# Kernel tuning notes

Measured on AMD Instinct MI355X. Metric: run time of the kernel, lower is better.

## Reference

```python
import jax, jax.numpy as jnp
import numpy as np

X, Y, Z, E, K, ITERS = 128, 128, 8, 64, 3, 3
XYZ = X * Y * Z
IMG_H, IMG_W = 384, 1280
FH, FW = 96, 320  # img_feat spatial size
LN_EPS = 1e-5
GRAD_SCALE = 0.1


def _homo_grid():
    # get_coordinates: meshgrid(arange(x), -arange(y), arange(z)), then append ones
    xs = (np.arange(X) * 0.8 + 0.0).astype(np.float32)
    ys = (-(np.arange(Y) * 0.8 - 51.2)).astype(np.float32)
    zs = (np.arange(Z) * 0.5 - 2.5).astype(np.float32)
    gx, gy, gz = np.meshgrid(xs, ys, zs, indexing='ij')
    g = np.stack([gx, gy, gz, np.ones_like(gx)], axis=-1)  # (X,Y,Z,4)
    return jnp.asarray(g)


def _grid_sample(img, grid):
    # F.grid_sample: bilinear, padding_mode='zeros', align_corners=False
    # img: (B,C,H,W), grid: (B,N,K,2) xy in [-1,1] -> out (B,C,N,K)
    B, C, H, W = img.shape
    x = ((grid[..., 0] + 1.0) * W - 1.0) * 0.5
    y = ((grid[..., 1] + 1.0) * H - 1.0) * 0.5
    x0 = jnp.floor(x); y0 = jnp.floor(y)
    x1 = x0 + 1.0; y1 = y0 + 1.0
    wx1 = x - x0; wx0 = 1.0 - wx1
    wy1 = y - y0; wy0 = 1.0 - wy1
    flat = img.reshape(B, C, H * W)

    def gather(xi, yi):
        valid = (xi >= 0) & (xi < W) & (yi >= 0) & (yi < H)  # (B,N,K)
        xi_c = jnp.clip(xi, 0, W - 1).astype(jnp.int32)
        yi_c = jnp.clip(yi, 0, H - 1).astype(jnp.int32)
        idx = yi_c * W + xi_c  # (B,N,K)
        g = jnp.take_along_axis(flat, idx.reshape(B, 1, -1), axis=2)
        g = g.reshape(B, C, idx.shape[1], idx.shape[2])
        return g * valid[:, None].astype(img.dtype)

    out = (gather(x0, y0) * (wx0 * wy0)[:, None]
           + gather(x1, y0) * (wx1 * wy0)[:, None]
           + gather(x0, y1) * (wx0 * wy1)[:, None]
           + gather(x1, y1) * (wx1 * wy1)[:, None])
    return out


def setup_inputs() -> dict:
    key = jax.random.key(0)
    ks = jax.random.split(key, 8)
    # realistic extrinsic (velo->cam) and intrinsic so projections land in-image
    T_velo2cam = jnp.array([[[0., -1., 0., 0.],
                             [0., 0., -1., -0.3],
                             [1., 0., 0., 0.5]]], dtype=jnp.float32)
    intrinsic = jnp.array([[[700., 0., 640.],
                            [0., 700., 192.],
                            [0., 0., 1.]]], dtype=jnp.float32)
    img_feat = jax.random.normal(ks[0], (1, E, FH, FW), jnp.float32)
    bev_embedding = 0.1 * jax.random.normal(ks[1], (X, Y, Z, E), jnp.float32)
    W_off = 0.02 * jax.random.normal(ks[2], (ITERS, E, 2 * K), jnp.float32)
    b_off = 0.02 * jax.random.normal(ks[3], (ITERS, 2 * K), jnp.float32)
    s_off = jnp.full((ITERS,), 0.1, jnp.float32)  # Scale(0.1)
    W_w = 0.02 * jax.random.normal(ks[4], (ITERS, E, K), jnp.float32)
    b_w = jnp.zeros((ITERS, K), jnp.float32)
    W_l = (E ** -0.5) * jax.random.normal(ks[5], (ITERS, E, E), jnp.float32)
    b_l = jnp.zeros((ITERS, E), jnp.float32)
    ln_g = jnp.ones((ITERS, E), jnp.float32)
    ln_b = jnp.zeros((ITERS, E), jnp.float32)
    return dict(T_velo2cam=T_velo2cam, intrinsic=intrinsic, img_feat=img_feat,
                bev_embedding=bev_embedding, W_off=W_off, b_off=b_off, s_off=s_off,
                W_w=W_w, b_w=b_w, W_l=W_l, b_l=b_l, ln_g=ln_g, ln_b=ln_b)


def reference(T_velo2cam, intrinsic, img_feat, bev_embedding,
              W_off, b_off, s_off, W_w, b_w, W_l, b_l, ln_g, ln_b):
    homo = _homo_grid()  # (X,Y,Z,4)
    T = jnp.einsum('bij,bjk->bik', intrinsic, T_velo2cam)  # (B,3,4)
    pts = jnp.einsum('bij,xyzj->bxyzi', T, homo)  # (B,X,Y,Z,3)
    uv = pts[..., 0:2] / pts[..., 2:3]
    half = jnp.array([IMG_W / 2.0, IMG_H / 2.0], pts.dtype)
    coord = (uv / half - 1.0).reshape(1, XYZ, 1, 2)  # (B,XYZ,1,2)
    bev = bev_embedding.reshape(1, XYZ, 1, E)
    for i in range(ITERS):
        off = (bev @ W_off[i] + b_off[i]) * s_off[i]  # Linear -> Scale
        # GradientScale(0.1): identity fwd, grad*0.1 bwd
        off = GRAD_SCALE * off + jax.lax.stop_gradient((1.0 - GRAD_SCALE) * off)
        off = off.reshape(1, XYZ, K, 2)
        w = jax.nn.softmax(bev @ W_w[i] + b_w[i], axis=-1)[:, :, 0, :]  # (1,XYZ,K)
        feat = _grid_sample(img_feat, coord + off)  # (1,E,XYZ,K)
        feat = jnp.sum(feat * w[:, None], axis=-1)  # (1,E,XYZ)
        bev = bev + jnp.transpose(feat, (0, 2, 1))[:, :, None, :]  # (1,XYZ,1,E)
        # LinearLNDropout (dropout inactive in eval)
        h = bev @ W_l[i] + b_l[i]
        mu = jnp.mean(h, axis=-1, keepdims=True)
        var = jnp.mean((h - mu) ** 2, axis=-1, keepdims=True)
        h = (h - mu) * jax.lax.rsqrt(var + LN_EPS) * ln_g[i] + ln_b[i]
        bev = bev + h
    bev = bev.reshape(1, X, Y, Z, E)
    return jnp.transpose(bev, (0, 4, 2, 1, 3)).mean(-1)  # (B,E,Y,X)
```

## Files before the change

### kernel.cpp

```cpp
#include <hip/hip_runtime.h>
#include <math.h>

#define XD 128
#define YD 128
#define ZD 8
#define ED 64
#define KD 3
#define NITER 3
#define FHD 96
#define FWD 320
#define HALF_W 640.0f
#define HALF_H 192.0f

#define ASTRIDE 80
#define DSTR 28
#define HSTRIDE 68

#define OFF_AB   0
#define OFF_SD   2560
#define OFF_SW   3328
#define OFF_DH   4096
#define OFF_CXY  8448
#define WAVE_LDS 8576

typedef __attribute__((ext_vector_type(8))) short short8;
typedef __attribute__((ext_vector_type(4))) float f32x4;

__device__ __forceinline__ unsigned short f2bf(float f) {
    unsigned u = __float_as_uint(f);
    u += 0x7fff + ((u >> 16) & 1);
    return (unsigned short)(u >> 16);
}

__global__ __launch_bounds__(256) void k_prep(const float* __restrict__ img,
                                              float* __restrict__ outHWC,
                                              const float* __restrict__ W_off,
                                              const float* __restrict__ W_w,
                                              const float* __restrict__ W_l,
                                              unsigned short* __restrict__ W9f,
                                              unsigned short* __restrict__ Wlf) {
    if (blockIdx.x < (FHD * FWD) / 64) {
        __shared__ float tile[64][65];
        const int hw0 = blockIdx.x * 64;
        const int lane = threadIdx.x & 63;
        const int r = threadIdx.x >> 6;
#pragma unroll
        for (int i = 0; i < 16; ++i) {
            int e = r + 4 * i;
            tile[e][lane] = img[e * (FHD * FWD) + hw0 + lane];
        }
        __syncthreads();
#pragma unroll
        for (int i = 0; i < 16; ++i) {
            int row = r + 4 * i;
            outHWC[(hw0 + row) * 64 + lane] = tile[lane][row];
        }
    } else {
        int idx = (blockIdx.x - (FHD * FWD) / 64) * 256 + threadIdx.x;
        if (idx < 3 * 4 * 2 * 64) {
            int lane = idx & 63, s = (idx >> 6) & 1, t = (idx >> 7) & 3, i = idx >> 9;
            int n = t * 16 + (lane & 15), quad = lane >> 4;
#pragma unroll
            for (int jj = 0; jj < 8; ++jj) {
                int ep = s * 32 + quad * 8 + jj;
                Wlf[idx * 8 + jj] = f2bf(W_l[(i * ED + ep) * ED + n]);
            }
        } else if (idx < 3 * 4 * 2 * 64 + 3 * 2 * 64) {
            int k = idx - 3 * 4 * 2 * 64;
            int lane = k & 63, s = (k >> 6) & 1, i = k >> 7;
            int n = lane & 15, quad = lane >> 4;
#pragma unroll
            for (int jj = 0; jj < 8; ++jj) {
                int ep = s * 32 + quad * 8 + jj;
                float v = 0.0f;
                if (n < 6) v = W_off[(i * ED + ep) * 6 + n];
                else if (n < 9) v = W_w[(i * ED + ep) * 3 + (n - 6)];
                W9f[k * 8 + jj] = f2bf(v);
            }
        }
    }
}

__global__ __launch_bounds__(256, 4) void k_main(
    const float* __restrict__ Tv,
    const float* __restrict__ intr,
    const float* __restrict__ imgHWC,
    const float* __restrict__ bev_in,
    const unsigned short* __restrict__ W9f,
    const unsigned short* __restrict__ Wlf,
    const float* __restrict__ b_off,
    const float* __restrict__ s_off,
    const float* __restrict__ b_w,
    const float* __restrict__ b_l,
    const float* __restrict__ ln_g,
    const float* __restrict__ ln_b,
    float* __restrict__ tmp)
{
    __shared__ __align__(16) char smem[4][WAVE_LDS];

    const int lane = threadIdx.x & 63;
    const int wv = threadIdx.x >> 6;
    const int wid2 = __builtin_amdgcn_readfirstlane(blockIdx.x * 4 + wv);
    const int m16 = lane & 15;
    const int quad = lane >> 4;

    char* base = smem[wv];
    unsigned short* Ab = (unsigned short*)(base + OFF_AB);
    int*   Sd  = (int*)(base + OFF_SD);
    float* Sw  = (float*)(base + OFF_SW);
    float* Db  = (float*)(base + OFF_DH);
    float* Hb  = (float*)(base + OFF_DH);
    float* Cxy = (float*)(base + OFF_CXY);

    float T[12];
#pragma unroll
    for (int r = 0; r < 3; ++r)
#pragma unroll
        for (int c = 0; c < 4; ++c)
            T[r * 4 + c] = intr[r * 3 + 0] * Tv[0 * 4 + c] +
                           intr[r * 3 + 1] * Tv[1 * 4 + c] +
                           intr[r * 3 + 2] * Tv[2 * 4 + c];

    float bev[16];
#pragma unroll
    for (int p = 0; p < 2; ++p) {
        int q = 2 * wid2 + p;
        int x = q & (XD - 1);
        int y = q >> 7;
        float gx = x * 0.8f;
        float gy = 51.2f - y * 0.8f;
        int pbase = (((x << 7) | y) << 9);
#pragma unroll
        for (int z = 0; z < ZD; ++z) {
            float gz = z * 0.5f - 2.5f;
            float p0 = T[0] * gx + T[1] * gy + T[2] * gz + T[3];
            float p1 = T[4] * gx + T[5] * gy + T[6] * gz + T[7];
            float p2 = T[8] * gx + T[9] * gy + T[10] * gz + T[11];
            float cxv = (p0 / p2) / HALF_W - 1.0f;
            float cyv = (p1 / p2) / HALF_H - 1.0f;
            int m = p * 8 + z;
            if (lane == 0) {
                Cxy[m * 2 + 0] = cxv;
                Cxy[m * 2 + 1] = cyv;
            }
            bev[m] = bev_in[pbase + z * ED + lane];
        }
    }

    for (int i = 0; i < NITER; ++i) {
#pragma unroll
        for (int m = 0; m < 16; ++m) Ab[m * ASTRIDE + lane] = f2bf(bev[m]);

        short8 wb0 = *(const short8*)(W9f + ((i * 2 + 0) * 64 + lane) * 8);
        short8 wb1 = *(const short8*)(W9f + ((i * 2 + 1) * 64 + lane) * 8);
        short8 a0 = *(const short8*)(Ab + m16 * ASTRIDE + quad * 8);
        short8 a1 = *(const short8*)(Ab + m16 * ASTRIDE + 32 + quad * 8);
        f32x4 dlog = {0.0f, 0.0f, 0.0f, 0.0f};
        dlog = __builtin_amdgcn_mfma_f32_16x16x32_bf16(a0, wb0, dlog, 0, 0, 0);
        dlog = __builtin_amdgcn_mfma_f32_16x16x32_bf16(a1, wb1, dlog, 0, 0, 0);
#pragma unroll
        for (int r = 0; r < 4; ++r) Db[(quad * 4 + r) * DSTR + m16] = dlog[r];

        const float so = s_off[i];
        const float bo0 = b_off[i * 6 + 0], bo1 = b_off[i * 6 + 1], bo2 = b_off[i * 6 + 2];
        const float bo3 = b_off[i * 6 + 3], bo4 = b_off[i * 6 + 4], bo5 = b_off[i * 6 + 5];
        const float bw0 = b_w[i * 3 + 0], bw1 = b_w[i * 3 + 1], bw2 = b_w[i * 3 + 2];

        if (lane < 48) {
            int m = lane / 3;
            int k = lane - m * 3;
            const float* Dm = Db + m * DSTR;
            float4 qa = *(const float4*)(Dm);
            float4 qb = *(const float4*)(Dm + 4);
            float l8 = Dm[8];

            float ox0 = (qa.x + bo0) * so, oy0 = (qa.y + bo1) * so;
            float ox1 = (qa.z + bo2) * so, oy1 = (qa.w + bo3) * so;
            float ox2 = (qb.x + bo4) * so, oy2 = (qb.y + bo5) * so;
            float l0 = qb.z + bw0, l1 = qb.w + bw1, l2 = l8 + bw2;
            float mx = fmaxf(fmaxf(l0, l1), l2);
            float e0 = __expf(l0 - mx), e1 = __expf(l1 - mx), e2 = __expf(l2 - mx);
            float inv = 1.0f / (e0 + e1 + e2);
            float wk0 = e0 * inv, wk1 = e1 * inv, wk2 = e2 * inv;

            float wkk = (k == 0) ? wk0 : ((k == 1) ? wk1 : wk2);
            float ox  = (k == 0) ? ox0 : ((k == 1) ? ox1 : ox2);
            float oy  = (k == 0) ? oy0 : ((k == 1) ? oy1 : oy2);

            float2 c = *(const float2*)(Cxy + m * 2);
            float gxx = c.x + ox, gyy = c.y + oy;
            float px = ((gxx + 1.0f) * (float)FWD - 1.0f) * 0.5f;
            float py = ((gyy + 1.0f) * (float)FHD - 1.0f) * 0.5f;
            float x0f = floorf(px), y0f = floorf(py);
            float fx = px - x0f, fy = py - y0f;
            int ix0 = (int)x0f, iy0 = (int)y0f;
            int ix1 = ix0 + 1, iy1 = iy0 + 1;
            float mx0 = (ix0 >= 0 && ix0 < FWD) ? 1.0f : 0.0f;
            float mx1 = (ix1 >= 0 && ix1 < FWD) ? 1.0f : 0.0f;
            float my0 = (iy0 >= 0 && iy0 < FHD) ? 1.0f : 0.0f;
            float my1 = (iy1 >= 0 && iy1 < FHD) ? 1.0f : 0.0f;
            int cx0 = min(max(ix0, 0), FWD - 1);
            int cx1 = min(max(ix1, 0), FWD - 1);
            int cy0 = min(max(iy0, 0), FHD - 1);
            int cy1 = min(max(iy1, 0), FHD - 1);
            int r0 = cy0 * FWD, r1 = cy1 * FWD;
            float wx1 = fx, wx0 = 1.0f - fx;
            float wy1 = fy, wy0 = 1.0f - fy;
            *(int4*)(Sd + lane * 4) =
                make_int4(r0 + cx0, r0 + cx1, r1 + cx0, r1 + cx1);
            *(float4*)(Sw + lane * 4) =
                make_float4(wkk * wx0 * wy0 * mx0 * my0, wkk * wx1 * wy0 * mx1 * my0,
                            wkk * wx0 * wy1 * mx0 * my1, wkk * wx1 * wy1 * mx1 * my1);
        }

        float b2[16];
#pragma unroll
        for (int m = 0; m < 16; ++m) {
            float feat = 0.0f;
#pragma unroll
            for (int k = 0; k < KD; ++k) {
                int s = m * 3 + k;
                int4 id = *(const int4*)(Sd + s * 4);
                float4 w4 = *(const float4*)(Sw + s * 4);
                feat = fmaf(w4.x, imgHWC[(id.x << 6) + lane], feat);
                feat = fmaf(w4.y, imgHWC[(id.y << 6) + lane], feat);
                feat = fmaf(w4.z, imgHWC[(id.z << 6) + lane], feat);
                feat = fmaf(w4.w, imgHWC[(id.w << 6) + lane], feat);
            }
            b2[m] = bev[m] + feat;
        }

#pragma unroll
        for (int m = 0; m < 16; ++m) Ab[m * ASTRIDE + lane] = f2bf(b2[m]);
        short8 a0b = *(const short8*)(Ab + m16 * ASTRIDE + quad * 8);
        short8 a1b = *(const short8*)(Ab + m16 * ASTRIDE + 32 + quad * 8);
        f32x4 accs[4];
#pragma unroll
        for (int t = 0; t < 4; ++t) {
            float bb = b_l[i * ED + t * 16 + m16];
            f32x4 acc = {bb, bb, bb, bb};
            short8 w0 = *(const short8*)(Wlf + (((i * 4 + t) * 2 + 0) * 64 + lane) * 8);
            short8 w1 = *(const short8*)(Wlf + (((i * 4 + t) * 2 + 1) * 64 + lane) * 8);
            acc = __builtin_amdgcn_mfma_f32_16x16x32_bf16(a0b, w0, acc, 0, 0, 0);
            acc = __builtin_amdgcn_mfma_f32_16x16x32_bf16(a1b, w1, acc, 0, 0, 0);
            accs[t] = acc;
        }

        float s1[4], s2[4];
#pragma unroll
        for (int r = 0; r < 4; ++r) {
            s1[r] = accs[0][r] + accs[1][r] + accs[2][r] + accs[3][r];
            s2[r] = accs[0][r] * accs[0][r];
            s2[r] = fmaf(accs[1][r], accs[1][r], s2[r]);
            s2[r] = fmaf(accs[2][r], accs[2][r], s2[r]);
            s2[r] = fmaf(accs[3][r], accs[3][r], s2[r]);
        }
#pragma unroll
        for (int d = 1; d <= 8; d <<= 1) {
#pragma unroll
            for (int r = 0; r < 4; ++r) {
                s1[r] += __shfl_xor(s1[r], d, 64);
                s2[r] += __shfl_xor(s2[r], d, 64);
            }
        }
        float gt[4], bt[4];
#pragma unroll
        for (int t = 0; t < 4; ++t) {
            gt[t] = ln_g[i * ED + t * 16 + m16];
            bt[t] = ln_b[i * ED + t * 16 + m16];
        }
#pragma unroll
        for (int r = 0; r < 4; ++r) {
            float mu = s1[r] * (1.0f / 64.0f);
            float var = fmaxf(s2[r] * (1.0f / 64.0f) - mu * mu, 0.0f);
            float rs = rsqrtf(var + 1e-5f);
            int row = quad * 4 + r;
#pragma unroll
            for (int t = 0; t < 4; ++t) {
                float hn = (accs[t][r] - mu) * rs * gt[t] + bt[t];
                Hb[row * HSTRIDE + t * 16 + m16] = hn;
            }
        }
#pragma unroll
        for (int m = 0; m < 16; ++m) bev[m] = b2[m] + Hb[m * HSTRIDE + lane];
    }

#pragma unroll
    for (int p = 0; p < 2; ++p) {
        float s = 0.0f;
#pragma unroll
        for (int z = 0; z < ZD; ++z) s += bev[p * 8 + z];
        tmp[(2 * wid2 + p) * ED + lane] = s * 0.125f;
    }
}

__global__ __launch_bounds__(256) void k_transpose(const float* __restrict__ tmp,
                                                   float* __restrict__ out) {
    __shared__ float tile[64][65];
    const int p0 = blockIdx.x * 64;
    const int lane = threadIdx.x & 63;
    const int r = threadIdx.x >> 6;
#pragma unroll
    for (int i = 0; i < 16; ++i) {
        int row = r + 4 * i;
        tile[row][lane] = tmp[(p0 + row) * ED + lane];
    }
    __syncthreads();
#pragma unroll
    for (int i = 0; i < 16; ++i) {
        int erow = r + 4 * i;
        out[erow * (YD * XD) + p0 + lane] = tile[lane][erow];
    }
}

extern "C" void kernel_launch(void* const* d_in, const int* in_sizes, int n_in,
                              void* d_out, int out_size, void* d_ws, size_t ws_size,
                              hipStream_t stream) {
    const float* Tv      = (const float*)d_in[0];
    const float* intr    = (const float*)d_in[1];
    const float* img     = (const float*)d_in[2];
    const float* bev_in  = (const float*)d_in[3];
    const float* W_off   = (const float*)d_in[4];
    const float* b_off   = (const float*)d_in[5];
    const float* s_off   = (const float*)d_in[6];
    const float* W_w     = (const float*)d_in[7];
    const float* b_w     = (const float*)d_in[8];
    const float* W_l     = (const float*)d_in[9];
    const float* b_l     = (const float*)d_in[10];
    const float* ln_g    = (const float*)d_in[11];
    const float* ln_b    = (const float*)d_in[12];
    float* out = (float*)d_out;

    char* ws = (char*)d_ws;
    float* imgHWC = (float*)ws;
    float* tmp = (float*)(ws + 7864320);
    unsigned short* W9f = (unsigned short*)(ws + 7864320 + 4194304);
    unsigned short* Wlf = (unsigned short*)(ws + 7864320 + 4194304 + 6144);

    k_prep<<<(FHD * FWD) / 64 + 8, 256, 0, stream>>>(img, imgHWC, W_off, W_w, W_l,
                                                     W9f, Wlf);
    k_main<<<(XD * YD / 2) / 4, 256, 0, stream>>>(Tv, intr, imgHWC, bev_in,
                                                  W9f, Wlf, b_off, s_off, b_w,
                                                  b_l, ln_g, ln_b, tmp);
    k_transpose<<<(YD * XD) / 64, 256, 0, stream>>>(tmp, out);
}
```

Measured before the change: 181.5 us.

## Fuse output transpose into main kernel and shrink per-wave LDS footprint

Removes the separate transpose kernel and its global tmp buffer. The main kernel now stages each block's 8 z-averaged outputs in shared memory and writes them directly in E-major layout. The per-wave LDS region is unified into one float buffer whose bf16 conversion happens at MFMA operand load time, which cuts LDS per block and may raise occupancy. The LayerNorm row reductions use DPP row shifts instead of shuffles. The costs are more pack instructions per A-operand load, a block-wide sync at the end, and small float2 output stores.

```diff
diff --git a/kernel.cpp b/kernel.cpp
--- a/kernel.cpp
+++ b/kernel.cpp
@@ -12,24 +12,51 @@
 #define HALF_W 640.0f
 #define HALF_H 192.0f
 
-#define ASTRIDE 80
+#define AFS  68
 #define DSTR 28
-#define HSTRIDE 68
-
-#define OFF_AB   0
-#define OFF_SD   2560
-#define OFF_SW   3328
-#define OFF_DH   4096
-#define OFF_CXY  8448
-#define WAVE_LDS 8576
+#define HSTR 66
+
+#define OFF_UNI  0
+#define OFF_SD   4352
+#define OFF_SW   5120
+#define OFF_CXY  5888
+#define WAVE_LDS 6016
 
 typedef __attribute__((ext_vector_type(8))) short short8;
 typedef __attribute__((ext_vector_type(4))) float f32x4;
+typedef float __attribute__((may_alias)) fal;
+typedef int   __attribute__((may_alias)) ial;
 
 __device__ __forceinline__ unsigned short f2bf(float f) {
     unsigned u = __float_as_uint(f);
     u += 0x7fff + ((u >> 16) & 1);
     return (unsigned short)(u >> 16);
+}
+
+__device__ __forceinline__ int packbf2(float f0, float f1) {
+    unsigned u0 = __float_as_uint(f0), u1 = __float_as_uint(f1);
+    u0 += 0x7fffu + ((u0 >> 16) & 1u);
+    u1 += 0x7fffu + ((u1 >> 16) & 1u);
+    return (int)((u0 >> 16) | (u1 & 0xffff0000u));
+}
+
+__device__ __forceinline__ short8 load_a(const fal* U, int row, int koff) {
+    f32x4 p0 = *(const f32x4*)(U + row * AFS + koff);
+    f32x4 p1 = *(const f32x4*)(U + row * AFS + koff + 4);
+    union { short8 s; int i[4]; } r;
+    r.i[0] = packbf2(p0[0], p0[1]);
+    r.i[1] = packbf2(p0[2], p0[3]);
+    r.i[2] = packbf2(p1[0], p1[1]);
+    r.i[3] = packbf2(p1[2], p1[3]);
+    return r.s;
+}
+
+__device__ __forceinline__ float rowsum16(float v) {
+    v += __int_as_float(__builtin_amdgcn_update_dpp(0, __float_as_int(v), 0x121, 0xf, 0xf, true));
+    v += __int_as_float(__builtin_amdgcn_update_dpp(0, __float_as_int(v), 0x122, 0xf, 0xf, true));
+    v += __int_as_float(__builtin_amdgcn_update_dpp(0, __float_as_int(v), 0x124, 0xf, 0xf, true));
+    v += __int_as_float(__builtin_amdgcn_update_dpp(0, __float_as_int(v), 0x128, 0xf, 0xf, true));
+    return v;
 }
 
 __global__ __launch_bounds__(256) void k_prep(const float* __restrict__ img,
@@ -94,9 +121,10 @@
     const float* __restrict__ b_l,
     const float* __restrict__ ln_g,
     const float* __restrict__ ln_b,
-    float* __restrict__ tmp)
+    float* __restrict__ out)
 {
-    __shared__ __align__(16) char smem[4][WAVE_LDS];
+    __shared__ __align__(16) char smem[4 * WAVE_LDS];
+    __shared__ __align__(16) float Ob[8][64];
 
     const int lane = threadIdx.x & 63;
     const int wv = threadIdx.x >> 6;
@@ -104,13 +132,11 @@
     const int m16 = lane & 15;
     const int quad = lane >> 4;
 
-    char* base = smem[wv];
-    unsigned short* Ab = (unsigned short*)(base + OFF_AB);
-    int*   Sd  = (int*)(base + OFF_SD);
-    float* Sw  = (float*)(base + OFF_SW);
-    float* Db  = (float*)(base + OFF_DH);
-    float* Hb  = (float*)(base + OFF_DH);
-    float* Cxy = (float*)(base + OFF_CXY);
+    char* base = smem + wv * WAVE_LDS;
+    fal*  U   = (fal*)(base + OFF_UNI);
+    ial*  Sd  = (ial*)(base + OFF_SD);
+    fal*  Sw  = (fal*)(base + OFF_SW);
+    fal*  Cxy = (fal*)(base + OFF_CXY);
 
     float T[12];
 #pragma unroll
@@ -149,17 +175,17 @@
 
     for (int i = 0; i < NITER; ++i) {
 #pragma unroll
-        for (int m = 0; m < 16; ++m) Ab[m * ASTRIDE + lane] = f2bf(bev[m]);
+        for (int m = 0; m < 16; ++m) U[m * AFS + lane] = bev[m];
 
         short8 wb0 = *(const short8*)(W9f + ((i * 2 + 0) * 64 + lane) * 8);
         short8 wb1 = *(const short8*)(W9f + ((i * 2 + 1) * 64 + lane) * 8);
-        short8 a0 = *(const short8*)(Ab + m16 * ASTRIDE + quad * 8);
-        short8 a1 = *(const short8*)(Ab + m16 * ASTRIDE + 32 + quad * 8);
+        short8 a0 = load_a(U, m16, quad * 8);
+        short8 a1 = load_a(U, m16, 32 + quad * 8);
         f32x4 dlog = {0.0f, 0.0f, 0.0f, 0.0f};
         dlog = __builtin_amdgcn_mfma_f32_16x16x32_bf16(a0, wb0, dlog, 0, 0, 0);
         dlog = __builtin_amdgcn_mfma_f32_16x16x32_bf16(a1, wb1, dlog, 0, 0, 0);
 #pragma unroll
-        for (int r = 0; r < 4; ++r) Db[(quad * 4 + r) * DSTR + m16] = dlog[r];
+        for (int r = 0; r < 4; ++r) U[(quad * 4 + r) * DSTR + m16] = dlog[r];
 
         const float so = s_off[i];
         const float bo0 = b_off[i * 6 + 0], bo1 = b_off[i * 6 + 1], bo2 = b_off[i * 6 + 2];
@@ -169,15 +195,15 @@
         if (lane < 48) {
             int m = lane / 3;
             int k = lane - m * 3;
-            const float* Dm = Db + m * DSTR;
-            float4 qa = *(const float4*)(Dm);
-            float4 qb = *(const float4*)(Dm + 4);
+            const fal* Dm = U + m * DSTR;
+            f32x4 qa = *(const f32x4*)(Dm);
+            f32x4 qb = *(const f32x4*)(Dm + 4);
             float l8 = Dm[8];
 
-            float ox0 = (qa.x + bo0) * so, oy0 = (qa.y + bo1) * so;
-            float ox1 = (qa.z + bo2) * so, oy1 = (qa.w + bo3) * so;
-            float ox2 = (qb.x + bo4) * so, oy2 = (qb.y + bo5) * so;
-            float l0 = qb.z + bw0, l1 = qb.w + bw1, l2 = l8 + bw2;
+            float ox0 = (qa[0] + bo0) * so, oy0 = (qa[1] + bo1) * so;
+            float ox1 = (qa[2] + bo2) * so, oy1 = (qa[3] + bo3) * so;
+            float ox2 = (qb[0] + bo4) * so, oy2 = (qb[1] + bo5) * so;
+            float l0 = qb[2] + bw0, l1 = qb[3] + bw1, l2 = l8 + bw2;
             float mx = fmaxf(fmaxf(l0, l1), l2);
             float e0 = __expf(l0 - mx), e1 = __expf(l1 - mx), e2 = __expf(l2 - mx);
             float inv = 1.0f / (e0 + e1 + e2);
@@ -187,8 +213,8 @@
             float ox  = (k == 0) ? ox0 : ((k == 1) ? ox1 : ox2);
             float oy  = (k == 0) ? oy0 : ((k == 1) ? oy1 : oy2);
 
-            float2 c = *(const float2*)(Cxy + m * 2);
-            float gxx = c.x + ox, gyy = c.y + oy;
+            float cxf = Cxy[m * 2 + 0], cyf = Cxy[m * 2 + 1];
+            float gxx = cxf + ox, gyy = cyf + oy;
             float px = ((gxx + 1.0f) * (float)FWD - 1.0f) * 0.5f;
             float py = ((gyy + 1.0f) * (float)FHD - 1.0f) * 0.5f;
             float x0f = floorf(px), y0f = floorf(py);
@@ -206,11 +232,13 @@
             int r0 = cy0 * FWD, r1 = cy1 * FWD;
             float wx1 = fx, wx0 = 1.0f - fx;
             float wy1 = fy, wy0 = 1.0f - fy;
-            *(int4*)(Sd + lane * 4) =
-                make_int4(r0 + cx0, r0 + cx1, r1 + cx0, r1 + cx1);
-            *(float4*)(Sw + lane * 4) =
-                make_float4(wkk * wx0 * wy0 * mx0 * my0, wkk * wx1 * wy0 * mx1 * my0,
-                            wkk * wx0 * wy1 * mx0 * my1, wkk * wx1 * wy1 * mx1 * my1);
+            ial* sd = Sd + lane * 4;
+            sd[0] = r0 + cx0; sd[1] = r0 + cx1; sd[2] = r1 + cx0; sd[3] = r1 + cx1;
+            fal* sw = Sw + lane * 4;
+            sw[0] = wkk * wx0 * wy0 * mx0 * my0;
+            sw[1] = wkk * wx1 * wy0 * mx1 * my0;
+            sw[2] = wkk * wx0 * wy1 * mx0 * my1;
+            sw[3] = wkk * wx1 * wy1 * mx1 * my1;
         }
 
         float b2[16];
@@ -222,18 +250,18 @@
                 int s = m * 3 + k;
                 int4 id = *(const int4*)(Sd + s * 4);
                 float4 w4 = *(const float4*)(Sw + s * 4);
-                feat = fmaf(w4.x, imgHWC[(id.x << 6) + lane], feat);
-                feat = fmaf(w4.y, imgHWC[(id.y << 6) + lane], feat);
-                feat = fmaf(w4.z, imgHWC[(id.z << 6) + lane], feat);
-                feat = fmaf(w4.w, imgHWC[(id.w << 6) + lane], feat);
+                feat = fmaf(w4.x, imgHWC[(unsigned)((id.x << 6) + lane)], feat);
+                feat = fmaf(w4.y, imgHWC[(unsigned)((id.y << 6) + lane)], feat);
+                feat = fmaf(w4.z, imgHWC[(unsigned)((id.z << 6) + lane)], feat);
+                feat = fmaf(w4.w, imgHWC[(unsigned)((id.w << 6) + lane)], feat);
             }
             b2[m] = bev[m] + feat;
         }
 
 #pragma unroll
-        for (int m = 0; m < 16; ++m) Ab[m * ASTRIDE + lane] = f2bf(b2[m]);
-        short8 a0b = *(const short8*)(Ab + m16 * ASTRIDE + quad * 8);
-        short8 a1b = *(const short8*)(Ab + m16 * ASTRIDE + 32 + quad * 8);
+        for (int m = 0; m < 16; ++m) U[m * AFS + lane] = b2[m];
+        short8 a0b = load_a(U, m16, quad * 8);
+        short8 a1b = load_a(U, m16, 32 + quad * 8);
         f32x4 accs[4];
 #pragma unroll
         for (int t = 0; t < 4; ++t) {
@@ -254,14 +282,8 @@
             s2[r] = fmaf(accs[1][r], accs[1][r], s2[r]);
             s2[r] = fmaf(accs[2][r], accs[2][r], s2[r]);
             s2[r] = fmaf(accs[3][r], accs[3][r], s2[r]);
-        }
-#pragma unroll
-        for (int d = 1; d <= 8; d <<= 1) {
-#pragma unroll
-            for (int r = 0; r < 4; ++r) {
-                s1[r] += __shfl_xor(s1[r], d, 64);
-                s2[r] += __shfl_xor(s2[r], d, 64);
-            }
+            s1[r] = rowsum16(s1[r]);
+            s2[r] = rowsum16(s2[r]);
         }
         float gt[4], bt[4];
 #pragma unroll
@@ -278,11 +300,11 @@
 #pragma unroll
             for (int t = 0; t < 4; ++t) {
                 float hn = (accs[t][r] - mu) * rs * gt[t] + bt[t];
-                Hb[row * HSTRIDE + t * 16 + m16] = hn;
-            }
-        }
-#pragma unroll
-        for (int m = 0; m < 16; ++m) bev[m] = b2[m] + Hb[m * HSTRIDE + lane];
+                U[row * HSTR + t * 16 + m16] = hn;
+            }
+        }
+#pragma unroll
+        for (int m = 0; m < 16; ++m) bev[m] = b2[m] + U[m * HSTR + lane];
     }
 
 #pragma unroll
@@ -290,26 +312,17 @@
         float s = 0.0f;
 #pragma unroll
         for (int z = 0; z < ZD; ++z) s += bev[p * 8 + z];
-        tmp[(2 * wid2 + p) * ED + lane] = s * 0.125f;
-    }
-}
-
-__global__ __launch_bounds__(256) void k_transpose(const float* __restrict__ tmp,
-                                                   float* __restrict__ out) {
-    __shared__ float tile[64][65];
-    const int p0 = blockIdx.x * 64;
-    const int lane = threadIdx.x & 63;
-    const int r = threadIdx.x >> 6;
-#pragma unroll
-    for (int i = 0; i < 16; ++i) {
-        int row = r + 4 * i;
-        tile[row][lane] = tmp[(p0 + row) * ED + lane];
+        Ob[wv * 2 + p][lane] = s * 0.125f;
     }
     __syncthreads();
-#pragma unroll
-    for (int i = 0; i < 16; ++i) {
-        int erow = r + 4 * i;
-        out[erow * (YD * XD) + p0 + lane] = tile[lane][erow];
+    {
+        const int q0 = __builtin_amdgcn_readfirstlane(blockIdx.x * 8);
+        int t = threadIdx.x;
+        int e = t >> 2, pr = t & 3;
+        float2 o;
+        o.x = Ob[2 * pr + 0][e];
+        o.y = Ob[2 * pr + 1][e];
+        *(float2*)(out + e * (YD * XD) + q0 + 2 * pr) = o;
     }
 }
 
@@ -333,14 +346,12 @@
 
     char* ws = (char*)d_ws;
     float* imgHWC = (float*)ws;
-    float* tmp = (float*)(ws + 7864320);
-    unsigned short* W9f = (unsigned short*)(ws + 7864320 + 4194304);
-    unsigned short* Wlf = (unsigned short*)(ws + 7864320 + 4194304 + 6144);
+    unsigned short* W9f = (unsigned short*)(ws + 7864320);
+    unsigned short* Wlf = (unsigned short*)(ws + 7864320 + 6144);
 
     k_prep<<<(FHD * FWD) / 64 + 8, 256, 0, stream>>>(img, imgHWC, W_off, W_w, W_l,
                                                      W9f, Wlf);
-    k_main<<<(XD * YD / 2) / 4, 256, 0, stream>>>(Tv, intr, imgHWC, bev_in,
-                                                  W9f, Wlf, b_off, s_off, b_w,
-                                                  b_l, ln_g, ln_b, tmp);
-    k_transpose<<<(YD * XD) / 64, 256, 0, stream>>>(tmp, out);
-}
+    k_main<<<(XD * YD) / 8, 256, 0, stream>>>(Tv, intr, imgHWC, bev_in,
+                                              W9f, Wlf, b_off, s_off, b_w,
+                                              b_l, ln_g, ln_b, out);
+}
```

Result: slower. 199.6 us (+10.0%).
